# Kernel optimization log

Measured on AMD Instinct MI355X. Metric: run time of the kernel, lower is better.

## Reference

```python
import jax, jax.numpy as jnp
import numpy as np

N = 100000      # nodes
E = 1200000     # edges
D_IN = 128      # input_dim
H = 64          # hidden_dim
OUT = 3         # output_dim
EPS = 1e-5      # BatchNorm eps


def setup_inputs() -> dict:
    key = jax.random.key(0)
    ks = jax.random.split(key, 24)
    w = lambda k, shape: jax.random.normal(k, shape, jnp.float32) * 0.05
    return {
        "x": jax.random.normal(ks[0], (N, D_IN), jnp.float32),
        "edge_index": jax.random.randint(ks[1], (2, E), 0, N, dtype=jnp.int32),
        "proj_W": w(ks[2], (H, D_IN)), "proj_b": w(ks[3], (H,)),
        "conv1_W": w(ks[4], (H, H)), "conv1_b": w(ks[5], (H,)),
        "bn1_g": jnp.ones((H,), jnp.float32), "bn1_b": w(ks[6], (H,)),
        "conv2_W": w(ks[7], (H, H)), "conv2_b": w(ks[8], (H,)),
        "bn2_g": jnp.ones((H,), jnp.float32), "bn2_b": w(ks[9], (H,)),
        "conv3_W": w(ks[10], (H, H)), "conv3_b": w(ks[11], (H,)),
        "bn3_g": jnp.ones((H,), jnp.float32), "bn3_b": w(ks[12], (H,)),
        "byp_W": w(ks[13], (OUT, D_IN)), "byp_b": w(ks[14], (OUT,)),
        "head_W": w(ks[15], (OUT, H + OUT)), "head_b": w(ks[16], (OUT,)),
    }


def reference(x, edge_index, proj_W, proj_b,
              conv1_W, conv1_b, bn1_g, bn1_b,
              conv2_W, conv2_b, bn2_g, bn2_b,
              conv3_W, conv3_b, bn3_g, bn3_b,
              byp_W, byp_b, head_W, head_b):
    n = x.shape[0]
    row, col = edge_index[0], edge_index[1]
    loop = jnp.arange(n, dtype=row.dtype)
    row_f = jnp.concatenate([row, loop])   # source (with self loops)
    col_f = jnp.concatenate([col, loop])   # target
    # symmetric GCN normalization: deg over targets of A+I, edge weight 1
    deg = jax.ops.segment_sum(jnp.ones(row_f.shape, jnp.float32), col_f, num_segments=n)
    dinv = jnp.where(deg > 0, jax.lax.rsqrt(deg), 0.0)
    norm = dinv[row_f] * dinv[col_f]       # [E+N]

    def gcn(h, W, b):
        h = h @ W.T                                    # transform then propagate
        msg = h[row_f] * norm[:, None]                 # gather + scale
        return jax.ops.segment_sum(msg, col_f, num_segments=n) + b

    def bn(h, g, b):
        # eval-mode BatchNorm1d: running_mean=0, running_var=1 buffers
        return h * (g / jnp.sqrt(1.0 + EPS)) + b

    h = x @ proj_W.T + proj_b
    idn = h
    h = jax.nn.relu(bn(gcn(h, conv1_W, conv1_b), bn1_g, bn1_b)) + idn  # dropout inactive (eval)
    idn = h
    h = jax.nn.relu(bn(gcn(h, conv2_W, conv2_b), bn2_g, bn2_b)) + idn
    h = jax.nn.relu(bn(gcn(h, conv3_W, conv3_b), bn3_g, bn3_b))

    byp = x @ byp_W.T + byp_b
    p = jnp.concatenate([h, byp], axis=1) @ head_W.T + head_b
    kappa = jnp.clip(p[:, 0] * 5.0 + 2.5, 0.2, 10.0)
    alpha = p[:, 1]
    tau = jnp.clip(p[:, 2] + 0.5, 0.05, 2.0)
    return jnp.stack([kappa, alpha, tau], axis=1)
```

## Files before the change

kernel.cpp:

```cpp
#include <hip/hip_runtime.h>
#include <hip/hip_fp16.h>

#define NN 100000
#define NE 1200000
#define NBUK ((NN + 127) / 128)
#define NCHUNK 512

typedef _Float16 h8 __attribute__((ext_vector_type(8)));
typedef float f32x4 __attribute__((ext_vector_type(4)));
typedef float f32x2 __attribute__((ext_vector_type(2)));

__global__ __launch_bounds__(256) void k_bucketA(const int* __restrict__ col,
                                                 int* __restrict__ blkcnt,
                                                 int* __restrict__ bcnt) {
    __shared__ int lh[NBUK];
    const int tid = threadIdx.x;
    const int per = (NE + NCHUNK - 1) / NCHUNK;
    const int e0 = blockIdx.x * per;
    const int e1 = (e0 + per < NE) ? (e0 + per) : NE;
    for (int i = tid; i < NBUK; i += 256) lh[i] = 0;
    __syncthreads();
    for (int e = e0 + tid; e < e1; e += 256)
        atomicAdd(&lh[col[e] >> 7], 1);
    __syncthreads();
    for (int b = tid; b < NBUK; b += 256) {
        int v = lh[b];
        blkcnt[b * NCHUNK + blockIdx.x] = v;
        if (v) atomicAdd(&bcnt[b], v);
    }
}

__global__ __launch_bounds__(1024) void k_scanAll(int* __restrict__ blkcnt,
                                                  int* __restrict__ bcnt) {
    __shared__ int s[1024];
    const int b = blockIdx.x, tid = threadIdx.x;
    if (b < NBUK) {
        int v = (tid < NCHUNK) ? blkcnt[b * NCHUNK + tid] : 0;
        s[tid] = v;
        __syncthreads();
        #pragma unroll
        for (int d = 1; d < 1024; d <<= 1) {
            int t = (tid >= d) ? s[tid - d] : 0;
            __syncthreads();
            s[tid] += t;
            __syncthreads();
        }
        if (tid < NCHUNK) blkcnt[b * NCHUNK + tid] = s[tid] - v;
    } else {
        int v = (tid < NBUK) ? bcnt[tid] : 0;
        s[tid] = v;
        __syncthreads();
        #pragma unroll
        for (int d = 1; d < 1024; d <<= 1) {
            int t = (tid >= d) ? s[tid - d] : 0;
            __syncthreads();
            s[tid] += t;
            __syncthreads();
        }
        if (tid < NBUK) bcnt[tid] = s[tid] - v;
        if (tid == 0) bcnt[NBUK] = NE;
    }
}

__global__ __launch_bounds__(256) void k_bucketB(const int* __restrict__ row,
                                                 const int* __restrict__ col,
                                                 const int* __restrict__ bbase,
                                                 const int* __restrict__ blkcnt,
                                                 unsigned* __restrict__ tmp) {
    __shared__ int lh[NBUK];
    const int tid = threadIdx.x;
    const int per = (NE + NCHUNK - 1) / NCHUNK;
    const int e0 = blockIdx.x * per;
    const int e1 = (e0 + per < NE) ? (e0 + per) : NE;
    for (int b = tid; b < NBUK; b += 256)
        lh[b] = bbase[b] + blkcnt[b * NCHUNK + blockIdx.x];
    __syncthreads();
    for (int e = e0 + tid; e < e1; e += 256) {
        int c = col[e], r = row[e];
        int pos = atomicAdd(&lh[c >> 7], 1);
        tmp[pos] = ((unsigned)r << 7) | (unsigned)(c & 127);
    }
}

__global__ __launch_bounds__(256) void k_build(const unsigned* __restrict__ tmp,
                                               const int* __restrict__ bbase,
                                               int* __restrict__ off,
                                               float* __restrict__ dinv,
                                               int* __restrict__ csr_row) {
    __shared__ int cnt[128], s[128], cur[128];
    const int b = blockIdx.x, tid = threadIdx.x;
    const int colBase = b << 7;
    const int nCols = (NN - colBase < 128) ? (NN - colBase) : 128;
    const int seg0 = bbase[b], seg1 = bbase[b + 1];
    if (tid < 128) cnt[tid] = 0;
    __syncthreads();
    for (int i = seg0 + tid; i < seg1; i += 256)
        atomicAdd(&cnt[tmp[i] & 127], 1);
    __syncthreads();
    if (tid < 128) s[tid] = cnt[tid];
    __syncthreads();
    #pragma unroll
    for (int d = 1; d < 128; d <<= 1) {
        int t = (tid < 128 && tid >= d) ? s[tid - d] : 0;
        __syncthreads();
        if (tid < 128) s[tid] += t;
        __syncthreads();
    }
    if (tid < nCols) {
        int exc = seg0 + s[tid] - cnt[tid];
        off[colBase + tid] = exc;
        cur[tid] = exc;
        dinv[colBase + tid] = rsqrtf((float)cnt[tid] + 1.0f);
    }
    if (b == 0 && tid == 0) off[NN] = NE;
    __syncthreads();
    for (int i = seg0 + tid; i < seg1; i += 256) {
        unsigned v = tmp[i];
        int pos = atomicAdd(&cur[v & 127u], 1);
        csr_row[pos] = (int)(v >> 7);
    }
}

__global__ __launch_bounds__(256) void k_gemmPC(const float* __restrict__ X,
                                                const float* __restrict__ W,
                                                const float* __restrict__ bias,
                                                _Float16* __restrict__ Yh,
                                                const float* __restrict__ bypW,
                                                const float* __restrict__ bypb,
                                                float* __restrict__ bypOut,
                                                const float* __restrict__ convW1,
                                                const float* __restrict__ dinv,
                                                unsigned char* __restrict__ Y8,
                                                int n_nodes) {
    constexpr int D = 128, RS = D + 8, KS = D / 32;
    constexpr int RS2 = 72;
    __shared__ _Float16 Xh[64 * RS];
    __shared__ _Float16 Wh[64 * RS];
    const int tid = threadIdx.x;
    const int n0 = blockIdx.x * 64;

    for (int i = tid; i < 64 * (D / 8); i += 256) {
        int j = i / (D / 8), d8 = (i % (D / 8)) * 8;
        const float4* wp = (const float4*)&W[j * D + d8];
        float4 w0 = wp[0], w1 = wp[1];
        h8 h = { (_Float16)w0.x, (_Float16)w0.y, (_Float16)w0.z, (_Float16)w0.w,
                 (_Float16)w1.x, (_Float16)w1.y, (_Float16)w1.z, (_Float16)w1.w };
        *(h8*)&Wh[j * RS + d8] = h;
    }
    for (int i = tid; i < 64 * (D / 8); i += 256) {
        int nl = i / (D / 8), d8 = (i % (D / 8)) * 8;
        int n = n0 + nl; if (n >= n_nodes) n = n_nodes - 1;
        const float4* xp = (const float4*)&X[(size_t)n * D + d8];
        float4 x0 = xp[0], x1 = xp[1];
        h8 h = { (_Float16)x0.x, (_Float16)x0.y, (_Float16)x0.z, (_Float16)x0.w,
                 (_Float16)x1.x, (_Float16)x1.y, (_Float16)x1.z, (_Float16)x1.w };
        *(h8*)&Xh[nl * RS + d8] = h;
    }
    __syncthreads();

    const int wid = tid >> 6, lane = tid & 63;
    const int lm = lane & 15, lq = lane >> 4;
    const int mBase = wid * 16;

    h8 bfrag[4][KS];
    #pragma unroll
    for (int t = 0; t < 4; ++t)
        #pragma unroll
        for (int s = 0; s < KS; ++s)
            bfrag[t][s] = *(const h8*)&Wh[(t * 16 + lm) * RS + s * 32 + lq * 8];

    h8 bfragB[KS];
    #pragma unroll
    for (int s = 0; s < KS; ++s) {
        if (lm < 3) {
            const float4* wp = (const float4*)&bypW[lm * D + s * 32 + lq * 8];
            float4 w0 = wp[0], w1 = wp[1];
            bfragB[s] = (h8){ (_Float16)w0.x, (_Float16)w0.y, (_Float16)w0.z, (_Float16)w0.w,
                              (_Float16)w1.x, (_Float16)w1.y, (_Float16)w1.z, (_Float16)w1.w };
        } else {
            bfragB[s] = (h8)(_Float16)0;
        }
    }

    f32x4 acc[5] = {};
    #pragma unroll
    for (int s = 0; s < KS; ++s) {
        h8 a = *(const h8*)&Xh[(mBase + lm) * RS + s * 32 + lq * 8];
        #pragma unroll
        for (int t = 0; t < 4; ++t)
            acc[t] = __builtin_amdgcn_mfma_f32_16x16x32_f16(a, bfrag[t][s], acc[t], 0, 0, 0);
        acc[4] = __builtin_amdgcn_mfma_f32_16x16x32_f16(a, bfragB[s], acc[4], 0, 0, 0);
    }

    float bb[4];
    #pragma unroll
    for (int t = 0; t < 4; ++t) bb[t] = bias[t * 16 + lm];
    float bypbv = (lm < 3) ? bypb[lm] : 0.f;
    const int nodeBase = n0 + mBase + lq * 4;

    __syncthreads();

    #pragma unroll
    for (int r = 0; r < 4; ++r) {
        int node = nodeBase + r;
        int nloc = mBase + lq * 4 + r;
        #pragma unroll
        for (int t = 0; t < 4; ++t) {
            _Float16 hv = (_Float16)(acc[t][r] + bb[t]);
            Xh[nloc * RS2 + t * 16 + lm] = hv;
            if (node < n_nodes)
                Yh[(size_t)node * 64 + t * 16 + lm] = hv;
        }
        if (node < n_nodes && lm < 3)
            bypOut[node * 3 + lm] = acc[4][r] + bypbv;
    }
    for (int i = tid; i < 64 * 8; i += 256) {
        int j = i >> 3, d8 = (i & 7) * 8;
        const float4* wp = (const float4*)&convW1[j * 64 + d8];
        float4 w0 = wp[0], w1 = wp[1];
        h8 h = { (_Float16)w0.x, (_Float16)w0.y, (_Float16)w0.z, (_Float16)w0.w,
                 (_Float16)w1.x, (_Float16)w1.y, (_Float16)w1.z, (_Float16)w1.w };
        *(h8*)&Wh[j * RS2 + d8] = h;
    }
    __syncthreads();

    h8 cfrag[4][2];
    #pragma unroll
    for (int t = 0; t < 4; ++t)
        #pragma unroll
        for (int s = 0; s < 2; ++s)
            cfrag[t][s] = *(const h8*)&Wh[(t * 16 + lm) * RS2 + s * 32 + lq * 8];

    f32x4 acc2[4] = {};
    #pragma unroll
    for (int s = 0; s < 2; ++s) {
        h8 a = *(const h8*)&Xh[(mBase + lm) * RS2 + s * 32 + lq * 8];
        #pragma unroll
        for (int t = 0; t < 4; ++t)
            acc2[t] = __builtin_amdgcn_mfma_f32_16x16x32_f16(a, cfrag[t][s], acc2[t], 0, 0, 0);
    }
    #pragma unroll
    for (int r = 0; r < 4; ++r) {
        int node = nodeBase + r;
        if (node < n_nodes) {
            float sdv = dinv[node];
            #pragma unroll
            for (int t = 0; t < 4; ++t) {
                float v = acc2[t][r] * sdv;
                int pk = __builtin_amdgcn_cvt_pk_fp8_f32(v, v, 0, false);
                Y8[(size_t)node * 64 + t * 16 + lm] = (unsigned char)(pk & 0xff);
            }
        }
    }
}

template<bool HEAD>
__global__ __launch_bounds__(256) void k_gather(const unsigned char* __restrict__ hB8,
                                                const float* __restrict__ dinv,
                                                const int* __restrict__ off,
                                                const int* __restrict__ csr_row,
                                                const float* __restrict__ convb,
                                                const float* __restrict__ bng,
                                                const float* __restrict__ bnb,
                                                _Float16* __restrict__ hA,
                                                const float* __restrict__ nextW,
                                                unsigned char* __restrict__ Y8,
                                                const float* __restrict__ byp,
                                                const float* __restrict__ headW,
                                                const float* __restrict__ headb,
                                                float* __restrict__ out) {
    constexpr int RS2 = 72;
    __shared__ _Float16 Ws[HEAD ? 1 : 64 * RS2];
    __shared__ _Float16 Hs[HEAD ? 1 : 32 * RS2];
    __shared__ float HWs[HEAD ? 204 : 1];
    const int tid = threadIdx.x;
    if constexpr (HEAD) {
        for (int i = tid; i < 204; i += 256)
            HWs[i] = (i < 201) ? headW[i] : headb[i - 201];
        __syncthreads();
    } else {
        for (int i = tid; i < 64 * 8; i += 256) {
            int j = i >> 3, d8 = (i & 7) * 8;
            const float4* wp = (const float4*)&nextW[j * 64 + d8];
            float4 w0 = wp[0], w1 = wp[1];
            h8 h = { (_Float16)w0.x, (_Float16)w0.y, (_Float16)w0.z, (_Float16)w0.w,
                     (_Float16)w1.x, (_Float16)w1.y, (_Float16)w1.z, (_Float16)w1.w };
            *(h8*)&Ws[j * RS2 + d8] = h;
        }
    }
    const int wid = tid >> 6, lane = tid & 63;
    const int nloc = wid * 8 + (lane >> 3);
    const int n = blockIdx.x * 32 + nloc;
    const int oct = lane & 7;
    const int f0 = oct * 8;
    const int ngb = lane & 56;

    const int e0 = off[n];
    const int deg = off[n + 1] - e0;

    const uint2* rows8 = (const uint2*)hB8;
    float acc[8] = {0, 0, 0, 0, 0, 0, 0, 0};
    {
        uint2 selfw = rows8[(size_t)n * 8 + oct];
        f32x2 p0 = __builtin_amdgcn_cvt_pk_f32_fp8(selfw.x, false);
        f32x2 p1 = __builtin_amdgcn_cvt_pk_f32_fp8(selfw.x, true);
        f32x2 p2 = __builtin_amdgcn_cvt_pk_f32_fp8(selfw.y, false);
        f32x2 p3 = __builtin_amdgcn_cvt_pk_f32_fp8(selfw.y, true);
        acc[0] += p0.x; acc[1] += p0.y; acc[2] += p1.x; acc[3] += p1.y;
        acc[4] += p2.x; acc[5] += p2.y; acc[6] += p3.x; acc[7] += p3.y;
    }
    for (int it = 0; it < deg; it += 16) {
        const int s0 = it + oct, s1 = it + 8 + oct;
        int i0 = csr_row[(s0 < deg) ? e0 + s0 : e0];
        int i1 = csr_row[(s1 < deg) ? e0 + s1 : e0];
        uint2 w[16];
        #pragma unroll
        for (int q = 0; q < 8; ++q) {
            int rq = __shfl(i0, ngb | q, 64);
            w[q] = rows8[(size_t)rq * 8 + oct];
            if (it + q >= deg) { w[q].x = 0; w[q].y = 0; }
        }
        #pragma unroll
        for (int q = 8; q < 16; ++q) {
            int rq = __shfl(i1, ngb | (q - 8), 64);
            w[q] = rows8[(size_t)rq * 8 + oct];
            if (it + q >= deg) { w[q].x = 0; w[q].y = 0; }
        }
        #pragma unroll
        for (int q = 0; q < 16; ++q) {
            f32x2 p0 = __builtin_amdgcn_cvt_pk_f32_fp8(w[q].x, false);
            f32x2 p1 = __builtin_amdgcn_cvt_pk_f32_fp8(w[q].x, true);
            f32x2 p2 = __builtin_amdgcn_cvt_pk_f32_fp8(w[q].y, false);
            f32x2 p3 = __builtin_amdgcn_cvt_pk_f32_fp8(w[q].y, true);
            acc[0] += p0.x; acc[1] += p0.y; acc[2] += p1.x; acc[3] += p1.y;
            acc[4] += p2.x; acc[5] += p2.y; acc[6] += p3.x; acc[7] += p3.y;
        }
    }

    const float dv = dinv[n];
    const float bnscale = rsqrtf(1.0f + 1e-5f);
    const float4 cb0 = *(const float4*)&convb[f0], cb1 = *(const float4*)&convb[f0 + 4];
    const float4 g0  = *(const float4*)&bng[f0],  g1  = *(const float4*)&bng[f0 + 4];
    const float4 b0_ = *(const float4*)&bnb[f0],  b1_ = *(const float4*)&bnb[f0 + 4];
    const float cb[8] = { cb0.x, cb0.y, cb0.z, cb0.w, cb1.x, cb1.y, cb1.z, cb1.w };
    const float gg[8] = { g0.x, g0.y, g0.z, g0.w, g1.x, g1.y, g1.z, g1.w };
    const float bb[8] = { b0_.x, b0_.y, b0_.z, b0_.w, b1_.x, b1_.y, b1_.z, b1_.w };
    float v[8];
    #pragma unroll
    for (int j = 0; j < 8; ++j)
        v[j] = fmaxf((acc[j] * dv + cb[j]) * (gg[j] * bnscale) + bb[j], 0.0f);

    if constexpr (!HEAD) {
        size_t o = ((size_t)n << 6) + f0;
        h8 old = *(const h8*)&hA[o];
        #pragma unroll
        for (int j = 0; j < 8; ++j) v[j] += (float)old[j];
        h8 res = { (_Float16)v[0], (_Float16)v[1], (_Float16)v[2], (_Float16)v[3],
                   (_Float16)v[4], (_Float16)v[5], (_Float16)v[6], (_Float16)v[7] };
        *(h8*)&hA[o] = res;
        *(h8*)&Hs[nloc * RS2 + f0] = res;
        __syncthreads();

        const int lm = lane & 15, lq = lane >> 4;
        const int mt = (wid & 1) * 16;
        const int nt = (wid >> 1) * 32;
        h8 afrag[2], bfrag[2][2];
        #pragma unroll
        for (int s = 0; s < 2; ++s)
            afrag[s] = *(const h8*)&Hs[(mt + lm) * RS2 + s * 32 + lq * 8];
        #pragma unroll
        for (int t = 0; t < 2; ++t)
            #pragma unroll
            for (int s = 0; s < 2; ++s)
                bfrag[t][s] = *(const h8*)&Ws[(nt + t * 16 + lm) * RS2 + s * 32 + lq * 8];
        f32x4 acc2[2] = {};
        #pragma unroll
        for (int s = 0; s < 2; ++s)
            #pragma unroll
            for (int t = 0; t < 2; ++t)
                acc2[t] = __builtin_amdgcn_mfma_f32_16x16x32_f16(afrag[s], bfrag[t][s], acc2[t], 0, 0, 0);
        const int nodeBase = blockIdx.x * 32 + mt + lq * 4;
        #pragma unroll
        for (int r = 0; r < 4; ++r) {
            int node = nodeBase + r;
            float sdv = dinv[node];
            #pragma unroll
            for (int t = 0; t < 2; ++t) {
                float vv = acc2[t][r] * sdv;
                int pk = __builtin_amdgcn_cvt_pk_fp8_f32(vv, vv, 0, false);
                Y8[(size_t)node * 64 + nt + t * 16 + lm] = (unsigned char)(pk & 0xff);
            }
        }
    } else {
        float p[3];
        #pragma unroll
        for (int o = 0; o < 3; ++o) {
            float t = 0.f;
            #pragma unroll
            for (int j = 0; j < 8; ++j) t += v[j] * HWs[o * 67 + f0 + j];
            p[o] = t;
        }
        #pragma unroll
        for (int mask = 1; mask < 8; mask <<= 1) {
            #pragma unroll
            for (int o = 0; o < 3; ++o) p[o] += __shfl_xor(p[o], mask, 64);
        }
        if (oct == 0) {
            float by0 = byp[n * 3], by1 = byp[n * 3 + 1], by2 = byp[n * 3 + 2];
            #pragma unroll
            for (int o = 0; o < 3; ++o)
                p[o] += by0 * HWs[o * 67 + 64] + by1 * HWs[o * 67 + 65] + by2 * HWs[o * 67 + 66]
                      + HWs[201 + o];
            float kappa = fminf(fmaxf(p[0] * 5.0f + 2.5f, 0.2f), 10.0f);
            float tau   = fminf(fmaxf(p[2] + 0.5f, 0.05f), 2.0f);
            out[(size_t)n * 3]     = kappa;
            out[(size_t)n * 3 + 1] = p[1];
            out[(size_t)n * 3 + 2] = tau;
        }
    }
}

extern "C" void kernel_launch(void* const* d_in, const int* in_sizes, int n_in,
                              void* d_out, int out_size, void* d_ws, size_t ws_size,
                              hipStream_t stream) {
    const float* x     = (const float*)d_in[0];
    const int*   ei    = (const int*)d_in[1];
    const int*   row   = ei;
    const int*   col   = ei + NE;
    const float* projW = (const float*)d_in[2];
    const float* projb = (const float*)d_in[3];
    const float* convW[3] = { (const float*)d_in[4], (const float*)d_in[8],  (const float*)d_in[12] };
    const float* convb[3] = { (const float*)d_in[5], (const float*)d_in[9],  (const float*)d_in[13] };
    const float* bng[3]   = { (const float*)d_in[6], (const float*)d_in[10], (const float*)d_in[14] };
    const float* bnb[3]   = { (const float*)d_in[7], (const float*)d_in[11], (const float*)d_in[15] };
    const float* bypW  = (const float*)d_in[16];
    const float* bypb  = (const float*)d_in[17];
    const float* headW = (const float*)d_in[18];
    const float* headb = (const float*)d_in[19];
    float* out = (float*)d_out;

    float*    ws   = (float*)d_ws;
    float*    dinv = ws;
    _Float16* hAh  = (_Float16*)(ws + 102400);
    unsigned char* hB8a = (unsigned char*)(hAh + (size_t)NN * 64);
    float*    byp  = (float*)(hB8a + (size_t)NN * 64);
    int*      off     = (int*)(byp + 300032);
    int*      csr_row = off + 100096;
    int*      bcnt    = csr_row + NE;
    int*      blkcnt  = bcnt + 784;
    unsigned char* hB8b = (unsigned char*)(blkcnt + (size_t)NBUK * NCHUNK);
    unsigned* tmp     = (unsigned*)hAh;

    hipMemsetAsync(bcnt, 0, 784 * sizeof(int), stream);
    k_bucketA<<<NCHUNK, 256, 0, stream>>>(col, blkcnt, bcnt);
    k_scanAll<<<NBUK + 1, 1024, 0, stream>>>(blkcnt, bcnt);
    k_bucketB<<<NCHUNK, 256, 0, stream>>>(row, col, bcnt, blkcnt, tmp);
    k_build<<<NBUK, 256, 0, stream>>>(tmp, bcnt, off, dinv, csr_row);

    k_gemmPC<<<(NN + 63) / 64, 256, 0, stream>>>(
        x, projW, projb, hAh, bypW, bypb, byp, convW[0], dinv, hB8a, NN);

    k_gather<false><<<NN / 32, 256, 0, stream>>>(
        hB8a, dinv, off, csr_row, convb[0], bng[0], bnb[0], hAh,
        convW[1], hB8b, nullptr, nullptr, nullptr, nullptr);
    k_gather<false><<<NN / 32, 256, 0, stream>>>(
        hB8b, dinv, off, csr_row, convb[1], bng[1], bnb[1], hAh,
        convW[2], hB8a, nullptr, nullptr, nullptr, nullptr);
    k_gather<true><<<NN / 32, 256, 0, stream>>>(
        hB8a, dinv, off, csr_row, convb[2], bng[2], bnb[2], nullptr,
        nullptr, nullptr, byp, headW, headb, out);
}
```

Baseline: 264.0 us.

## Fuse bucketing with projection GEMM and conv1 transform into CSR build

Merges the edge-bucket histogram and the input projection GEMM into one launch, with block index deciding the role, and drops the memset. Bucket totals are now prefix-scanned inside the scatter and build kernels. The first conv transform (H @ W1 scaled by dinv, stored as FP8) moves into the CSR build kernel, so it no longer needs dinv from a separate pass. The gather loop is reworked to load neighbour indices directly in groups of 8, with the loop bound set to the max degree across each group's lanes. This cuts kernel launches and serial dependencies, at the cost of redundant per-block prefix sums, extra shared memory, and a separate tmp buffer.

```diff
diff --git a/kernel.cpp b/kernel.cpp
--- a/kernel.cpp
+++ b/kernel.cpp
@@ -5,143 +5,46 @@
 #define NE 1200000
 #define NBUK ((NN + 127) / 128)
 #define NCHUNK 512
+#define NPROJ ((NN + 63) / 64)
 
 typedef _Float16 h8 __attribute__((ext_vector_type(8)));
 typedef float f32x4 __attribute__((ext_vector_type(4)));
 typedef float f32x2 __attribute__((ext_vector_type(2)));
 
-__global__ __launch_bounds__(256) void k_bucketA(const int* __restrict__ col,
-                                                 int* __restrict__ blkcnt,
-                                                 int* __restrict__ bcnt) {
-    __shared__ int lh[NBUK];
-    const int tid = threadIdx.x;
-    const int per = (NE + NCHUNK - 1) / NCHUNK;
-    const int e0 = blockIdx.x * per;
-    const int e1 = (e0 + per < NE) ? (e0 + per) : NE;
-    for (int i = tid; i < NBUK; i += 256) lh[i] = 0;
-    __syncthreads();
-    for (int e = e0 + tid; e < e1; e += 256)
-        atomicAdd(&lh[col[e] >> 7], 1);
-    __syncthreads();
-    for (int b = tid; b < NBUK; b += 256) {
-        int v = lh[b];
-        blkcnt[b * NCHUNK + blockIdx.x] = v;
-        if (v) atomicAdd(&bcnt[b], v);
-    }
-}
-
-__global__ __launch_bounds__(1024) void k_scanAll(int* __restrict__ blkcnt,
-                                                  int* __restrict__ bcnt) {
-    __shared__ int s[1024];
-    const int b = blockIdx.x, tid = threadIdx.x;
-    if (b < NBUK) {
-        int v = (tid < NCHUNK) ? blkcnt[b * NCHUNK + tid] : 0;
-        s[tid] = v;
-        __syncthreads();
-        #pragma unroll
-        for (int d = 1; d < 1024; d <<= 1) {
-            int t = (tid >= d) ? s[tid - d] : 0;
-            __syncthreads();
-            s[tid] += t;
-            __syncthreads();
-        }
-        if (tid < NCHUNK) blkcnt[b * NCHUNK + tid] = s[tid] - v;
-    } else {
-        int v = (tid < NBUK) ? bcnt[tid] : 0;
-        s[tid] = v;
-        __syncthreads();
-        #pragma unroll
-        for (int d = 1; d < 1024; d <<= 1) {
-            int t = (tid >= d) ? s[tid - d] : 0;
-            __syncthreads();
-            s[tid] += t;
-            __syncthreads();
-        }
-        if (tid < NBUK) bcnt[tid] = s[tid] - v;
-        if (tid == 0) bcnt[NBUK] = NE;
-    }
-}
-
-__global__ __launch_bounds__(256) void k_bucketB(const int* __restrict__ row,
-                                                 const int* __restrict__ col,
-                                                 const int* __restrict__ bbase,
-                                                 const int* __restrict__ blkcnt,
-                                                 unsigned* __restrict__ tmp) {
-    __shared__ int lh[NBUK];
-    const int tid = threadIdx.x;
-    const int per = (NE + NCHUNK - 1) / NCHUNK;
-    const int e0 = blockIdx.x * per;
-    const int e1 = (e0 + per < NE) ? (e0 + per) : NE;
-    for (int b = tid; b < NBUK; b += 256)
-        lh[b] = bbase[b] + blkcnt[b * NCHUNK + blockIdx.x];
-    __syncthreads();
-    for (int e = e0 + tid; e < e1; e += 256) {
-        int c = col[e], r = row[e];
-        int pos = atomicAdd(&lh[c >> 7], 1);
-        tmp[pos] = ((unsigned)r << 7) | (unsigned)(c & 127);
-    }
-}
-
-__global__ __launch_bounds__(256) void k_build(const unsigned* __restrict__ tmp,
-                                               const int* __restrict__ bbase,
-                                               int* __restrict__ off,
-                                               float* __restrict__ dinv,
-                                               int* __restrict__ csr_row) {
-    __shared__ int cnt[128], s[128], cur[128];
-    const int b = blockIdx.x, tid = threadIdx.x;
-    const int colBase = b << 7;
-    const int nCols = (NN - colBase < 128) ? (NN - colBase) : 128;
-    const int seg0 = bbase[b], seg1 = bbase[b + 1];
-    if (tid < 128) cnt[tid] = 0;
-    __syncthreads();
-    for (int i = seg0 + tid; i < seg1; i += 256)
-        atomicAdd(&cnt[tmp[i] & 127], 1);
-    __syncthreads();
-    if (tid < 128) s[tid] = cnt[tid];
-    __syncthreads();
-    #pragma unroll
-    for (int d = 1; d < 128; d <<= 1) {
-        int t = (tid < 128 && tid >= d) ? s[tid - d] : 0;
-        __syncthreads();
-        if (tid < 128) s[tid] += t;
-        __syncthreads();
-    }
-    if (tid < nCols) {
-        int exc = seg0 + s[tid] - cnt[tid];
-        off[colBase + tid] = exc;
-        cur[tid] = exc;
-        dinv[colBase + tid] = rsqrtf((float)cnt[tid] + 1.0f);
-    }
-    if (b == 0 && tid == 0) off[NN] = NE;
-    __syncthreads();
-    for (int i = seg0 + tid; i < seg1; i += 256) {
-        unsigned v = tmp[i];
-        int pos = atomicAdd(&cur[v & 127u], 1);
-        csr_row[pos] = (int)(v >> 7);
-    }
-}
-
-__global__ __launch_bounds__(256) void k_gemmPC(const float* __restrict__ X,
-                                                const float* __restrict__ W,
-                                                const float* __restrict__ bias,
-                                                _Float16* __restrict__ Yh,
+__global__ __launch_bounds__(256) void k_fusedA(const int* __restrict__ col,
+                                                int* __restrict__ blkcnt,
+                                                const float* __restrict__ X,
+                                                const float* __restrict__ projW,
+                                                const float* __restrict__ projb,
                                                 const float* __restrict__ bypW,
                                                 const float* __restrict__ bypb,
-                                                float* __restrict__ bypOut,
-                                                const float* __restrict__ convW1,
-                                                const float* __restrict__ dinv,
-                                                unsigned char* __restrict__ Y8,
-                                                int n_nodes) {
+                                                _Float16* __restrict__ Yh,
+                                                float* __restrict__ bypOut) {
     constexpr int D = 128, RS = D + 8, KS = D / 32;
-    constexpr int RS2 = 72;
     __shared__ _Float16 Xh[64 * RS];
     __shared__ _Float16 Wh[64 * RS];
     const int tid = threadIdx.x;
-    const int n0 = blockIdx.x * 64;
+
+    if (blockIdx.x < NCHUNK) {
+        int* lh = (int*)Xh;
+        const int per = (NE + NCHUNK - 1) / NCHUNK;
+        const int e0 = blockIdx.x * per;
+        const int e1 = (e0 + per < NE) ? (e0 + per) : NE;
+        for (int i = tid; i < NBUK; i += 256) lh[i] = 0;
+        __syncthreads();
+        for (int e = e0 + tid; e < e1; e += 256)
+            atomicAdd(&lh[col[e] >> 7], 1);
+        __syncthreads();
+        for (int b = tid; b < NBUK; b += 256)
+            blkcnt[b * NCHUNK + blockIdx.x] = lh[b];
+        return;
+    }
+
+    const int n0 = (blockIdx.x - NCHUNK) * 64;
 
     for (int i = tid; i < 64 * (D / 8); i += 256) {
         int j = i / (D / 8), d8 = (i % (D / 8)) * 8;
-        const float4* wp = (const float4*)&W[j * D + d8];
+        const float4* wp = (const float4*)&projW[j * D + d8];
         float4 w0 = wp[0], w1 = wp[1];
         h8 h = { (_Float16)w0.x, (_Float16)w0.y, (_Float16)w0.z, (_Float16)w0.w,
                  (_Float16)w1.x, (_Float16)w1.y, (_Float16)w1.z, (_Float16)w1.w };
@@ -149,7 +52,7 @@
     }
     for (int i = tid; i < 64 * (D / 8); i += 256) {
         int nl = i / (D / 8), d8 = (i % (D / 8)) * 8;
-        int n = n0 + nl; if (n >= n_nodes) n = n_nodes - 1;
+        int n = n0 + nl; if (n >= NN) n = NN - 1;
         const float4* xp = (const float4*)&X[(size_t)n * D + d8];
         float4 x0 = xp[0], x1 = xp[1];
         h8 h = { (_Float16)x0.x, (_Float16)x0.y, (_Float16)x0.z, (_Float16)x0.w,
@@ -194,61 +97,191 @@
 
     float bb[4];
     #pragma unroll
-    for (int t = 0; t < 4; ++t) bb[t] = bias[t * 16 + lm];
+    for (int t = 0; t < 4; ++t) bb[t] = projb[t * 16 + lm];
     float bypbv = (lm < 3) ? bypb[lm] : 0.f;
     const int nodeBase = n0 + mBase + lq * 4;
 
-    __syncthreads();
-
     #pragma unroll
     for (int r = 0; r < 4; ++r) {
         int node = nodeBase + r;
-        int nloc = mBase + lq * 4 + r;
-        #pragma unroll
-        for (int t = 0; t < 4; ++t) {
-            _Float16 hv = (_Float16)(acc[t][r] + bb[t]);
-            Xh[nloc * RS2 + t * 16 + lm] = hv;
-            if (node < n_nodes)
-                Yh[(size_t)node * 64 + t * 16 + lm] = hv;
-        }
-        if (node < n_nodes && lm < 3)
-            bypOut[node * 3 + lm] = acc[4][r] + bypbv;
+        if (node < NN) {
+            #pragma unroll
+            for (int t = 0; t < 4; ++t)
+                Yh[(size_t)node * 64 + t * 16 + lm] = (_Float16)(acc[t][r] + bb[t]);
+            if (lm < 3)
+                bypOut[node * 3 + lm] = acc[4][r] + bypbv;
+        }
+    }
+}
+
+__global__ __launch_bounds__(1024) void k_scanAll(int* __restrict__ blkcnt,
+                                                  int* __restrict__ bcnt) {
+    __shared__ int s[1024];
+    const int b = blockIdx.x, tid = threadIdx.x;
+    int v = (tid < NCHUNK) ? blkcnt[b * NCHUNK + tid] : 0;
+    s[tid] = v;
+    __syncthreads();
+    #pragma unroll
+    for (int d = 1; d < 1024; d <<= 1) {
+        int t = (tid >= d) ? s[tid - d] : 0;
+        __syncthreads();
+        s[tid] += t;
+        __syncthreads();
+    }
+    if (tid < NCHUNK) blkcnt[b * NCHUNK + tid] = s[tid] - v;
+    if (tid == 1023) bcnt[b] = s[1023];
+}
+
+__global__ __launch_bounds__(256) void k_bucketB(const int* __restrict__ row,
+                                                 const int* __restrict__ col,
+                                                 const int* __restrict__ bcnt,
+                                                 const int* __restrict__ blkcnt,
+                                                 unsigned* __restrict__ tmp) {
+    __shared__ int lh[NBUK];
+    __shared__ int part[256];
+    const int tid = threadIdx.x;
+    int loc[4]; int sum = 0;
+    #pragma unroll
+    for (int j = 0; j < 4; ++j) {
+        int idx = tid * 4 + j;
+        loc[j] = sum;
+        sum += (idx < NBUK) ? bcnt[idx] : 0;
+    }
+    part[tid] = sum;
+    __syncthreads();
+    #pragma unroll
+    for (int d = 1; d < 256; d <<= 1) {
+        int t = (tid >= d) ? part[tid - d] : 0;
+        __syncthreads();
+        part[tid] += t;
+        __syncthreads();
+    }
+    const int excl = part[tid] - sum;
+    #pragma unroll
+    for (int j = 0; j < 4; ++j) {
+        int idx = tid * 4 + j;
+        if (idx < NBUK)
+            lh[idx] = excl + loc[j] + blkcnt[idx * NCHUNK + blockIdx.x];
+    }
+    __syncthreads();
+    const int per = (NE + NCHUNK - 1) / NCHUNK;
+    const int e0 = blockIdx.x * per;
+    const int e1 = (e0 + per < NE) ? (e0 + per) : NE;
+    for (int e = e0 + tid; e < e1; e += 256) {
+        int c = col[e], r = row[e];
+        int pos = atomicAdd(&lh[c >> 7], 1);
+        tmp[pos] = ((unsigned)r << 7) | (unsigned)(c & 127);
+    }
+}
+
+__global__ __launch_bounds__(256) void k_buildM(const unsigned* __restrict__ tmp,
+                                                const int* __restrict__ bcnt,
+                                                int* __restrict__ off,
+                                                float* __restrict__ dinv,
+                                                int* __restrict__ csr_row,
+                                                const _Float16* __restrict__ hA,
+                                                const float* __restrict__ W1,
+                                                unsigned char* __restrict__ Y8) {
+    constexpr int RS2 = 72;
+    __shared__ int cnt[128], s[128], cur[128];
+    __shared__ int red[256];
+    __shared__ float dinvL[128];
+    __shared__ _Float16 Hs[128 * RS2];
+    __shared__ _Float16 WsL[64 * RS2];
+    const int b = blockIdx.x, tid = threadIdx.x;
+
+    for (int i = tid; i < 128 * 8; i += 256) {
+        int j = i >> 3, d8 = (i & 7) * 8;
+        int n = (b << 7) + j; if (n >= NN) n = NN - 1;
+        *(h8*)&Hs[j * RS2 + d8] = *(const h8*)&hA[(size_t)n * 64 + d8];
     }
     for (int i = tid; i < 64 * 8; i += 256) {
         int j = i >> 3, d8 = (i & 7) * 8;
-        const float4* wp = (const float4*)&convW1[j * 64 + d8];
+        const float4* wp = (const float4*)&W1[j * 64 + d8];
         float4 w0 = wp[0], w1 = wp[1];
         h8 h = { (_Float16)w0.x, (_Float16)w0.y, (_Float16)w0.z, (_Float16)w0.w,
                  (_Float16)w1.x, (_Float16)w1.y, (_Float16)w1.z, (_Float16)w1.w };
-        *(h8*)&Wh[j * RS2 + d8] = h;
-    }
-    __syncthreads();
-
+        *(h8*)&WsL[j * RS2 + d8] = h;
+    }
+
+    int ssum = 0;
+    for (int i = tid; i < b; i += 256) ssum += bcnt[i];
+    red[tid] = ssum;
+    __syncthreads();
+    #pragma unroll
+    for (int d = 128; d > 0; d >>= 1) {
+        if (tid < d) red[tid] += red[tid + d];
+        __syncthreads();
+    }
+    const int seg0 = red[0];
+    const int seg1 = seg0 + bcnt[b];
+    const int colBase = b << 7;
+    const int nCols = (NN - colBase < 128) ? (NN - colBase) : 128;
+    if (tid < 128) cnt[tid] = 0;
+    __syncthreads();
+    for (int i = seg0 + tid; i < seg1; i += 256)
+        atomicAdd(&cnt[tmp[i] & 127], 1);
+    __syncthreads();
+    if (tid < 128) s[tid] = cnt[tid];
+    __syncthreads();
+    #pragma unroll
+    for (int d = 1; d < 128; d <<= 1) {
+        int t = (tid < 128 && tid >= d) ? s[tid - d] : 0;
+        __syncthreads();
+        if (tid < 128) s[tid] += t;
+        __syncthreads();
+    }
+    if (tid < 128) {
+        float dv = rsqrtf((float)cnt[tid] + 1.0f);
+        dinvL[tid] = dv;
+        if (tid < nCols) {
+            int exc = seg0 + s[tid] - cnt[tid];
+            off[colBase + tid] = exc;
+            cur[tid] = exc;
+            dinv[colBase + tid] = dv;
+        }
+    }
+    if (b == 0 && tid == 0) off[NN] = NE;
+    __syncthreads();
+    for (int i = seg0 + tid; i < seg1; i += 256) {
+        unsigned v = tmp[i];
+        int pos = atomicAdd(&cur[v & 127u], 1);
+        csr_row[pos] = (int)(v >> 7);
+    }
+    __syncthreads();
+
+    const int wid = tid >> 6, lane = tid & 63;
+    const int lm = lane & 15, lq = lane >> 4;
+    const int mBase = wid * 16;
     h8 cfrag[4][2];
     #pragma unroll
     for (int t = 0; t < 4; ++t)
         #pragma unroll
-        for (int s = 0; s < 2; ++s)
-            cfrag[t][s] = *(const h8*)&Wh[(t * 16 + lm) * RS2 + s * 32 + lq * 8];
-
-    f32x4 acc2[4] = {};
-    #pragma unroll
-    for (int s = 0; s < 2; ++s) {
-        h8 a = *(const h8*)&Xh[(mBase + lm) * RS2 + s * 32 + lq * 8];
-        #pragma unroll
-        for (int t = 0; t < 4; ++t)
-            acc2[t] = __builtin_amdgcn_mfma_f32_16x16x32_f16(a, cfrag[t][s], acc2[t], 0, 0, 0);
-    }
-    #pragma unroll
-    for (int r = 0; r < 4; ++r) {
-        int node = nodeBase + r;
-        if (node < n_nodes) {
-            float sdv = dinv[node];
-            #pragma unroll
-            for (int t = 0; t < 4; ++t) {
-                float v = acc2[t][r] * sdv;
-                int pk = __builtin_amdgcn_cvt_pk_fp8_f32(v, v, 0, false);
-                Y8[(size_t)node * 64 + t * 16 + lm] = (unsigned char)(pk & 0xff);
+        for (int sx = 0; sx < 2; ++sx)
+            cfrag[t][sx] = *(const h8*)&WsL[(t * 16 + lm) * RS2 + sx * 32 + lq * 8];
+    #pragma unroll
+    for (int hh = 0; hh < 2; ++hh) {
+        const int rb = hh * 64 + mBase;
+        f32x4 acc2[4] = {};
+        #pragma unroll
+        for (int sx = 0; sx < 2; ++sx) {
+            h8 a = *(const h8*)&Hs[(rb + lm) * RS2 + sx * 32 + lq * 8];
+            #pragma unroll
+            for (int t = 0; t < 4; ++t)
+                acc2[t] = __builtin_amdgcn_mfma_f32_16x16x32_f16(a, cfrag[t][sx], acc2[t], 0, 0, 0);
+        }
+        #pragma unroll
+        for (int r = 0; r < 4; ++r) {
+            int nl = rb + lq * 4 + r;
+            int node = colBase + nl;
+            if (node < NN) {
+                float sdv = dinvL[nl];
+                #pragma unroll
+                for (int t = 0; t < 4; ++t) {
+                    float v = acc2[t][r] * sdv;
+                    int pk = __builtin_amdgcn_cvt_pk_fp8_f32(v, v, 0, false);
+                    Y8[(size_t)node * 64 + t * 16 + lm] = (unsigned char)(pk & 0xff);
+                }
             }
         }
     }
@@ -293,15 +326,20 @@
     const int n = blockIdx.x * 32 + nloc;
     const int oct = lane & 7;
     const int f0 = oct * 8;
-    const int ngb = lane & 56;
 
     const int e0 = off[n];
     const int deg = off[n + 1] - e0;
+    int m = deg;
+    #pragma unroll
+    for (int mask = 8; mask < 64; mask <<= 1) {
+        int o = __shfl_xor(m, mask, 64);
+        m = (o > m) ? o : m;
+    }
 
     const uint2* rows8 = (const uint2*)hB8;
     float acc[8] = {0, 0, 0, 0, 0, 0, 0, 0};
+    uint2 selfw = rows8[(size_t)n * 8 + oct];
     {
-        uint2 selfw = rows8[(size_t)n * 8 + oct];
         f32x2 p0 = __builtin_amdgcn_cvt_pk_f32_fp8(selfw.x, false);
         f32x2 p1 = __builtin_amdgcn_cvt_pk_f32_fp8(selfw.x, true);
         f32x2 p2 = __builtin_amdgcn_cvt_pk_f32_fp8(selfw.y, false);
@@ -309,25 +347,17 @@
         acc[0] += p0.x; acc[1] += p0.y; acc[2] += p1.x; acc[3] += p1.y;
         acc[4] += p2.x; acc[5] += p2.y; acc[6] += p3.x; acc[7] += p3.y;
     }
-    for (int it = 0; it < deg; it += 16) {
-        const int s0 = it + oct, s1 = it + 8 + oct;
-        int i0 = csr_row[(s0 < deg) ? e0 + s0 : e0];
-        int i1 = csr_row[(s1 < deg) ? e0 + s1 : e0];
-        uint2 w[16];
+    for (int it = 0; it < m; it += 8) {
+        uint2 w[8];
         #pragma unroll
         for (int q = 0; q < 8; ++q) {
-            int rq = __shfl(i0, ngb | q, 64);
+            bool vq = it + q < deg;
+            int rq = csr_row[vq ? e0 + it + q : 0];
             w[q] = rows8[(size_t)rq * 8 + oct];
-            if (it + q >= deg) { w[q].x = 0; w[q].y = 0; }
-        }
-        #pragma unroll
-        for (int q = 8; q < 16; ++q) {
-            int rq = __shfl(i1, ngb | (q - 8), 64);
-            w[q] = rows8[(size_t)rq * 8 + oct];
-            if (it + q >= deg) { w[q].x = 0; w[q].y = 0; }
-        }
-        #pragma unroll
-        for (int q = 0; q < 16; ++q) {
+            if (!vq) { w[q].x = 0; w[q].y = 0; }
+        }
+        #pragma unroll
+        for (int q = 0; q < 8; ++q) {
             f32x2 p0 = __builtin_amdgcn_cvt_pk_f32_fp8(w[q].x, false);
             f32x2 p1 = __builtin_amdgcn_cvt_pk_f32_fp8(w[q].x, true);
             f32x2 p2 = __builtin_amdgcn_cvt_pk_f32_fp8(w[q].y, false);
@@ -449,16 +479,14 @@
     int*      bcnt    = csr_row + NE;
     int*      blkcnt  = bcnt + 784;
     unsigned char* hB8b = (unsigned char*)(blkcnt + (size_t)NBUK * NCHUNK);
-    unsigned* tmp     = (unsigned*)hAh;
-
-    hipMemsetAsync(bcnt, 0, 784 * sizeof(int), stream);
-    k_bucketA<<<NCHUNK, 256, 0, stream>>>(col, blkcnt, bcnt);
-    k_scanAll<<<NBUK + 1, 1024, 0, stream>>>(blkcnt, bcnt);
+    unsigned* tmp     = (unsigned*)(hB8b + (size_t)NN * 64);
+
+    k_fusedA<<<NCHUNK + NPROJ, 256, 0, stream>>>(
+        col, blkcnt, x, projW, projb, bypW, bypb, hAh, byp);
+    k_scanAll<<<NBUK, 1024, 0, stream>>>(blkcnt, bcnt);
     k_bucketB<<<NCHUNK, 256, 0, stream>>>(row, col, bcnt, blkcnt, tmp);
-    k_build<<<NBUK, 256, 0, stream>>>(tmp, bcnt, off, dinv, csr_row);
-
-    k_gemmPC<<<(NN + 63) / 64, 256, 0, stream>>>(
-        x, projW, projb, hAh, bypW, bypb, byp, convW[0], dinv, hB8a, NN);
+    k_buildM<<<NBUK, 256, 0, stream>>>(tmp, bcnt, off, dinv, csr_row,
+                                       hAh, convW[0], hB8a);
 
     k_gather<false><<<NN / 32, 256, 0, stream>>>(
         hB8a, dinv, off, csr_row, convb[0], bng[0], bnb[0], hAh,
```

Result: faster. 251.8 us (-4.6%).
